# Kernel tuning notes

Measured on AMD Instinct MI355X. Metric: run time of the kernel, lower is better.

## Reference

```python
import jax, jax.numpy as jnp
import numpy as np

N = 10000
K1, K2 = 10, 25
DIM = 64
OUT = 128
NUM_GRAPHS = 64


def setup_inputs() -> dict:
    key = jax.random.key(0)
    ks = jax.random.split(key, 10)
    h0 = jax.random.normal(ks[0], (N, DIM), jnp.float32)
    h1 = jax.random.normal(ks[1], (N * K1, DIM), jnp.float32)
    h2 = jax.random.normal(ks[2], (N * K1 * K2, DIM), jnp.float32)
    # glorot-ish scaled weights
    w0 = jax.random.normal(ks[3], (2 * DIM, OUT), jnp.float32) * (2.0 / (2 * DIM + OUT)) ** 0.5
    b0 = jnp.zeros((OUT,), jnp.float32)
    w1 = jax.random.normal(ks[4], (2 * OUT, OUT), jnp.float32) * (2.0 / (3 * OUT)) ** 0.5
    b1 = jnp.zeros((OUT,), jnp.float32)
    wr1 = jax.random.normal(ks[5], (OUT, 35), jnp.float32) * (2.0 / (OUT + 35)) ** 0.5
    br1 = jnp.zeros((35,), jnp.float32)
    wr2 = jax.random.normal(ks[6], (35, 35), jnp.float32) * (2.0 / 70) ** 0.5
    br2 = jnp.zeros((35,), jnp.float32)
    wr3 = jax.random.normal(ks[7], (35, 1), jnp.float32) * (2.0 / 36) ** 0.5
    br3 = jnp.zeros((1,), jnp.float32)
    states_graph_ids = jnp.sort(jax.random.randint(ks[8], (N,), 0, NUM_GRAPHS, jnp.int32))
    return {
        "h0": h0, "h1": h1, "h2": h2,
        "w0": w0, "b0": b0, "w1": w1, "b1": b1,
        "wr1": wr1, "br1": br1, "wr2": wr2, "br2": br2, "wr3": wr3, "br3": br3,
        "states_graph_ids": states_graph_ids, "num_graphs": NUM_GRAPHS,
    }


def _aggr_mean(src, neigh, w, b):
    # GraphSAGE mean aggregator: concat(src, mean(neighbors)) @ w + b, relu
    n, d = src.shape
    k = neigh.shape[0] // n
    neigh_mean = neigh.reshape(n, k, d).mean(axis=1)  # (n, d)
    return jax.nn.relu(jnp.concatenate([src, neigh_mean], axis=1) @ w + b)


def reference(h0, h1, h2, w0, b0, w1, b1, wr1, br1, wr2, br2, wr3, br3,
              states_graph_ids, num_graphs):
    # round 0: shared aggregator across depths
    a01 = _aggr_mean(h0, h1, w0, b0)          # (N, OUT)
    a12 = _aggr_mean(h1, h2, w0, b0)          # (N*K1, OUT)
    # round 1
    out = _aggr_mean(a01, a12, w1, b1)        # (N, OUT)
    # segment_sum over sorted graph ids
    seg = jax.ops.segment_sum(out, states_graph_ids, num_segments=num_graphs,
                              indices_are_sorted=True)  # (G, OUT)
    # readout MLP (dropout inactive at inference)
    r = jax.nn.selu(seg @ wr1 + br1)
    r = jax.nn.selu(r @ wr2 + br2)
    r = r @ wr3 + br3                          # (G, 1)
    return r
```

## Files before the change

kernel.cpp:

```cpp
#include <hip/hip_runtime.h>
#include <hip/hip_bf16.h>
#include <math.h>

#define N_NODES 10000
#define K1 10
#define K2 25
#define DIM 64
#define OUT 128
#define NGRAPH 64

__global__ __launch_bounds__(256, 4) void kA(const float* __restrict__ h1,
                                             const float* __restrict__ h2,
                                             const float* __restrict__ w0,
                                             const float* __restrict__ b0,
                                             float* __restrict__ a12mean)
{
    __shared__ float  xbuf[K1][2 * DIM];
    __shared__ float4 red4[16][16];
    __shared__ float  pbuf[K1][OUT];

    const int t    = threadIdx.x;
    const int node = blockIdx.x;
    const int c    = t & 127;
    const int h    = t >> 7;

    float w0r[64];
#pragma unroll
    for (int k = 0; k < 64; ++k)
        w0r[k] = w0[(h * 64 + k) * OUT + c];
    const float b0r = b0[c];

    {
        const float* h1b = h1 + (size_t)node * (K1 * DIM);
        for (int idx = t; idx < K1 * DIM; idx += 256)
            xbuf[idx >> 6][idx & 63] = h1b[idx];
    }

    const int cc = t & 15;
    const int sl = t >> 4;
    const float4* h2b = (const float4*)h2 + (size_t)node * (K1 * K2 * DIM / 4);
    for (int j = 0; j < K1; ++j) {
        const float4* bj = h2b + j * (K2 * DIM / 4);
        float4 s = bj[sl * 16 + cc];
        if (sl < 9) {
            float4 s2 = bj[(sl + 16) * 16 + cc];
            s.x += s2.x; s.y += s2.y; s.z += s2.z; s.w += s2.w;
        }
        red4[sl][cc] = s;
        __syncthreads();
        if (t < 64) {
            const float* rf = (const float*)red4;
            float sum = 0.f;
#pragma unroll
            for (int ss = 0; ss < 16; ++ss) sum += rf[ss * 64 + t];
            xbuf[j][DIM + t] = sum * (1.0f / K2);
        }
        __syncthreads();
    }

    float myp[K1];
#pragma unroll
    for (int j = 0; j < K1; ++j) {
        const float4* xj = (const float4*)(&xbuf[j][h * DIM]);
        float p = 0.f;
#pragma unroll
        for (int k4 = 0; k4 < 16; ++k4) {
            float4 xv = xj[k4];
            p += xv.x * w0r[4 * k4 + 0];
            p += xv.y * w0r[4 * k4 + 1];
            p += xv.z * w0r[4 * k4 + 2];
            p += xv.w * w0r[4 * k4 + 3];
        }
        if (h == 1) pbuf[j][c] = p;
        else        myp[j]     = p;
    }
    __syncthreads();
    if (h == 0) {
        float acc = 0.f;
#pragma unroll
        for (int j = 0; j < K1; ++j) {
            float y = myp[j] + pbuf[j][c] + b0r;
            acc += (y > 0.f ? y : 0.f);
        }
        a12mean[(size_t)node * OUT + c] = acc * (1.0f / K1);
    }
}

__global__ __launch_bounds__(256, 2) void kB(const float* __restrict__ h0,
                                             const float* __restrict__ h1,
                                             const float* __restrict__ w0,
                                             const float* __restrict__ b0,
                                             const float* __restrict__ w1,
                                             const float* __restrict__ b1,
                                             const float* __restrict__ a12mean,
                                             const int*   __restrict__ gids,
                                             float* __restrict__ seg)
{
    __shared__ float x0[16][2 * DIM];
    __shared__ float x1[16][2 * OUT];
    __shared__ float pbuf[16][OUT];

    const int t  = threadIdx.x;
    const int n0 = blockIdx.x * 16;
    const int c  = t & 127;
    const int hh = t >> 7;

    float w0r[64];
#pragma unroll
    for (int k = 0; k < 64; ++k)
        w0r[k] = w0[(hh * 64 + k) * OUT + c];
    const float b0r = b0[c];

    for (int idx = t; idx < 16 * DIM; idx += 256)
        x0[idx >> 6][idx & 63] = h0[(size_t)n0 * DIM + idx];

    {
        const int col = t & 63, isub = t >> 6;
        for (int chunk = 0; chunk < 4; ++chunk) {
            const int il = chunk * 4 + isub;
            const float* b = h1 + (size_t)(n0 + il) * (K1 * DIM);
            float s = 0.f;
#pragma unroll
            for (int r = 0; r < K1; ++r) s += b[r * DIM + col];
            x0[il][DIM + col] = s * (1.0f / K1);
        }
    }

    for (int idx = t; idx < 16 * OUT; idx += 256)
        x1[idx >> 7][OUT + (idx & 127)] = a12mean[(size_t)n0 * OUT + idx];
    __syncthreads();

    float myp[16];
#pragma unroll
    for (int i = 0; i < 16; ++i) {
        const float4* xi = (const float4*)(&x0[i][hh * DIM]);
        float p = 0.f;
#pragma unroll
        for (int k4 = 0; k4 < 16; ++k4) {
            float4 xv = xi[k4];
            p += xv.x * w0r[4 * k4 + 0] + xv.y * w0r[4 * k4 + 1]
               + xv.z * w0r[4 * k4 + 2] + xv.w * w0r[4 * k4 + 3];
        }
        if (hh == 1) pbuf[i][c] = p; else myp[i] = p;
    }
    __syncthreads();
    if (hh == 0) {
#pragma unroll
        for (int i = 0; i < 16; ++i) {
            float y = myp[i] + pbuf[i][c] + b0r;
            x1[i][c] = (y > 0.f ? y : 0.f);
        }
    }

    float w1r[128];
#pragma unroll
    for (int k = 0; k < 128; ++k)
        w1r[k] = w1[(hh * 128 + k) * OUT + c];
    const float b1r = b1[c];
    __syncthreads();

#pragma unroll
    for (int i = 0; i < 16; ++i) {
        const float4* xi = (const float4*)(&x1[i][hh * OUT]);
        float p = 0.f;
#pragma unroll
        for (int k4 = 0; k4 < 32; ++k4) {
            float4 xv = xi[k4];
            p += xv.x * w1r[4 * k4 + 0] + xv.y * w1r[4 * k4 + 1]
               + xv.z * w1r[4 * k4 + 2] + xv.w * w1r[4 * k4 + 3];
        }
        if (hh == 1) pbuf[i][c] = p; else myp[i] = p;
    }
    __syncthreads();
    if (hh == 0) {
        int   runGid = gids[n0];
        float runSum = 0.f;
#pragma unroll
        for (int i = 0; i < 16; ++i) {
            float y = myp[i] + pbuf[i][c] + b1r;
            y = (y > 0.f ? y : 0.f);
            const int g = gids[n0 + i];
            if (g != runGid) {
                atomicAdd(&seg[runGid * OUT + c], runSum);
                runSum = 0.f; runGid = g;
            }
            runSum += y;
        }
        atomicAdd(&seg[runGid * OUT + c], runSum);
    }
}

__global__ void kC(const float* __restrict__ seg,
                   const float* __restrict__ wr1, const float* __restrict__ br1,
                   const float* __restrict__ wr2, const float* __restrict__ br2,
                   const float* __restrict__ wr3, const float* __restrict__ br3,
                   float* __restrict__ out)
{
    __shared__ float r1[35], r2[35];
    const int g = blockIdx.x, l = threadIdx.x;
    const float* s = seg + (size_t)g * OUT;
    const float SCALE = 1.0507009873554805f;
    const float ALPHA = 1.6732632423543772f;

    if (l < 35) {
        float d = br1[l];
        for (int k = 0; k < OUT; ++k) d += s[k] * wr1[k * 35 + l];
        r1[l] = d > 0.f ? SCALE * d : SCALE * ALPHA * (expf(d) - 1.f);
    }
    __syncthreads();
    if (l < 35) {
        float d = br2[l];
        for (int k = 0; k < 35; ++k) d += r1[k] * wr2[k * 35 + l];
        r2[l] = d > 0.f ? SCALE * d : SCALE * ALPHA * (expf(d) - 1.f);
    }
    __syncthreads();
    if (l == 0) {
        float d = br3[0];
        for (int k = 0; k < 35; ++k) d += r2[k] * wr3[k];
        out[g] = d;
    }
}

extern "C" void kernel_launch(void* const* d_in, const int* in_sizes, int n_in,
                              void* d_out, int out_size, void* d_ws, size_t ws_size,
                              hipStream_t stream)
{
    const float* h0  = (const float*)d_in[0];
    const float* h1  = (const float*)d_in[1];
    const float* h2  = (const float*)d_in[2];
    const float* w0  = (const float*)d_in[3];
    const float* b0  = (const float*)d_in[4];
    const float* w1  = (const float*)d_in[5];
    const float* b1  = (const float*)d_in[6];
    const float* wr1 = (const float*)d_in[7];
    const float* br1 = (const float*)d_in[8];
    const float* wr2 = (const float*)d_in[9];
    const float* br2 = (const float*)d_in[10];
    const float* wr3 = (const float*)d_in[11];
    const float* br3 = (const float*)d_in[12];
    const int*  gids = (const int*)d_in[13];

    float* a12mean = (float*)d_ws;
    float* seg     = a12mean + (size_t)N_NODES * OUT;
    float* out     = (float*)d_out;

    hipMemsetAsync(seg, 0, NGRAPH * OUT * sizeof(float), stream);
    kA<<<N_NODES, 256, 0, stream>>>(h1, h2, w0, b0, a12mean);
    kB<<<N_NODES / 16, 256, 0, stream>>>(h0, h1, w0, b0, w1, b1, a12mean, gids, seg);
    kC<<<NGRAPH, 64, 0, stream>>>(seg, wr1, br1, wr2, br2, wr3, br3, out);
}
```

Baseline: 925.9 us.

## Fuse both aggregation stages into one kernel with split-K register GEMV

```diff
diff --git a/kernel.cpp b/kernel.cpp
--- a/kernel.cpp
+++ b/kernel.cpp
@@ -1,5 +1,4 @@
 #include <hip/hip_runtime.h>
-#include <hip/hip_bf16.h>
 #include <math.h>
 
 #define N_NODES 10000
@@ -9,184 +8,157 @@
 #define OUT 128
 #define NGRAPH 64
 
-__global__ __launch_bounds__(256, 4) void kA(const float* __restrict__ h1,
-                                             const float* __restrict__ h2,
-                                             const float* __restrict__ w0,
-                                             const float* __restrict__ b0,
-                                             float* __restrict__ a12mean)
+#define NPB 2
+#define RPB (NPB * K1)
+#define XROWS (RPB + NPB)
+#define QP 36
+#define XPITCH (4 * QP)
+#define QP1 68
+#define X1PITCH (4 * QP1)
+
+__global__ __launch_bounds__(256, 4) void kFused(
+    const float* __restrict__ h0, const float* __restrict__ h1,
+    const float* __restrict__ h2, const float* __restrict__ w0,
+    const float* __restrict__ b0, const float* __restrict__ w1,
+    const float* __restrict__ b1, const int* __restrict__ gids,
+    float* __restrict__ seg)
 {
-    __shared__ float  xbuf[K1][2 * DIM];
-    __shared__ float4 red4[16][16];
-    __shared__ float  pbuf[K1][OUT];
-
-    const int t    = threadIdx.x;
-    const int node = blockIdx.x;
-    const int c    = t & 127;
-    const int h    = t >> 7;
-
-    float w0r[64];
-#pragma unroll
-    for (int k = 0; k < 64; ++k)
-        w0r[k] = w0[(h * 64 + k) * OUT + c];
-    const float b0r = b0[c];
-
-    {
-        const float* h1b = h1 + (size_t)node * (K1 * DIM);
-        for (int idx = t; idx < K1 * DIM; idx += 256)
-            xbuf[idx >> 6][idx & 63] = h1b[idx];
-    }
-
-    const int cc = t & 15;
-    const int sl = t >> 4;
-    const float4* h2b = (const float4*)h2 + (size_t)node * (K1 * K2 * DIM / 4);
-    for (int j = 0; j < K1; ++j) {
-        const float4* bj = h2b + j * (K2 * DIM / 4);
-        float4 s = bj[sl * 16 + cc];
-        if (sl < 9) {
-            float4 s2 = bj[(sl + 16) * 16 + cc];
-            s.x += s2.x; s.y += s2.y; s.z += s2.z; s.w += s2.w;
-        }
-        red4[sl][cc] = s;
-        __syncthreads();
-        if (t < 64) {
-            const float* rf = (const float*)red4;
-            float sum = 0.f;
-#pragma unroll
-            for (int ss = 0; ss < 16; ++ss) sum += rf[ss * 64 + t];
-            xbuf[j][DIM + t] = sum * (1.0f / K2);
-        }
-        __syncthreads();
-    }
-
-    float myp[K1];
-#pragma unroll
-    for (int j = 0; j < K1; ++j) {
-        const float4* xj = (const float4*)(&xbuf[j][h * DIM]);
-        float p = 0.f;
-#pragma unroll
-        for (int k4 = 0; k4 < 16; ++k4) {
-            float4 xv = xj[k4];
-            p += xv.x * w0r[4 * k4 + 0];
-            p += xv.y * w0r[4 * k4 + 1];
-            p += xv.z * w0r[4 * k4 + 2];
-            p += xv.w * w0r[4 * k4 + 3];
-        }
-        if (h == 1) pbuf[j][c] = p;
-        else        myp[j]     = p;
-    }
-    __syncthreads();
-    if (h == 0) {
-        float acc = 0.f;
-#pragma unroll
-        for (int j = 0; j < K1; ++j) {
-            float y = myp[j] + pbuf[j][c] + b0r;
-            acc += (y > 0.f ? y : 0.f);
-        }
-        a12mean[(size_t)node * OUT + c] = acc * (1.0f / K1);
-    }
-}
-
-__global__ __launch_bounds__(256, 2) void kB(const float* __restrict__ h0,
-                                             const float* __restrict__ h1,
-                                             const float* __restrict__ w0,
-                                             const float* __restrict__ b0,
-                                             const float* __restrict__ w1,
-                                             const float* __restrict__ b1,
-                                             const float* __restrict__ a12mean,
-                                             const int*   __restrict__ gids,
-                                             float* __restrict__ seg)
-{
-    __shared__ float x0[16][2 * DIM];
-    __shared__ float x1[16][2 * OUT];
-    __shared__ float pbuf[16][OUT];
+    __shared__ float xbuf[XROWS][XPITCH];
+    __shared__ float x1p[NPB][X1PITCH];
 
     const int t  = threadIdx.x;
-    const int n0 = blockIdx.x * 16;
-    const int c  = t & 127;
-    const int hh = t >> 7;
-
-    float w0r[64];
-#pragma unroll
-    for (int k = 0; k < 64; ++k)
-        w0r[k] = w0[(hh * 64 + k) * OUT + c];
-    const float b0r = b0[c];
-
-    for (int idx = t; idx < 16 * DIM; idx += 256)
-        x0[idx >> 6][idx & 63] = h0[(size_t)n0 * DIM + idx];
-
-    {
-        const int col = t & 63, isub = t >> 6;
-        for (int chunk = 0; chunk < 4; ++chunk) {
-            const int il = chunk * 4 + isub;
-            const float* b = h1 + (size_t)(n0 + il) * (K1 * DIM);
-            float s = 0.f;
-#pragma unroll
-            for (int r = 0; r < K1; ++r) s += b[r * DIM + col];
-            x0[il][DIM + col] = s * (1.0f / K1);
-        }
-    }
-
-    for (int idx = t; idx < 16 * OUT; idx += 256)
-        x1[idx >> 7][OUT + (idx & 127)] = a12mean[(size_t)n0 * OUT + idx];
-    __syncthreads();
-
-    float myp[16];
-#pragma unroll
-    for (int i = 0; i < 16; ++i) {
-        const float4* xi = (const float4*)(&x0[i][hh * DIM]);
-        float p = 0.f;
-#pragma unroll
-        for (int k4 = 0; k4 < 16; ++k4) {
-            float4 xv = xi[k4];
-            p += xv.x * w0r[4 * k4 + 0] + xv.y * w0r[4 * k4 + 1]
-               + xv.z * w0r[4 * k4 + 2] + xv.w * w0r[4 * k4 + 3];
-        }
-        if (hh == 1) pbuf[i][c] = p; else myp[i] = p;
-    }
-    __syncthreads();
-    if (hh == 0) {
-#pragma unroll
-        for (int i = 0; i < 16; ++i) {
-            float y = myp[i] + pbuf[i][c] + b0r;
-            x1[i][c] = (y > 0.f ? y : 0.f);
-        }
-    }
-
-    float w1r[128];
-#pragma unroll
-    for (int k = 0; k < 128; ++k)
-        w1r[k] = w1[(hh * 128 + k) * OUT + c];
-    const float b1r = b1[c];
-    __syncthreads();
-
-#pragma unroll
-    for (int i = 0; i < 16; ++i) {
-        const float4* xi = (const float4*)(&x1[i][hh * OUT]);
-        float p = 0.f;
-#pragma unroll
-        for (int k4 = 0; k4 < 32; ++k4) {
-            float4 xv = xi[k4];
-            p += xv.x * w1r[4 * k4 + 0] + xv.y * w1r[4 * k4 + 1]
-               + xv.z * w1r[4 * k4 + 2] + xv.w * w1r[4 * k4 + 3];
-        }
-        if (hh == 1) pbuf[i][c] = p; else myp[i] = p;
-    }
-    __syncthreads();
-    if (hh == 0) {
-        int   runGid = gids[n0];
-        float runSum = 0.f;
-#pragma unroll
-        for (int i = 0; i < 16; ++i) {
-            float y = myp[i] + pbuf[i][c] + b1r;
-            y = (y > 0.f ? y : 0.f);
-            const int g = gids[n0 + i];
-            if (g != runGid) {
-                atomicAdd(&seg[runGid * OUT + c], runSum);
-                runSum = 0.f; runGid = g;
+    const int w  = t >> 6;
+    const int l  = t & 63;
+    const int kq = l & 3;
+    const int cp = l >> 2;
+    const int c0 = w * 32 + cp * 2;
+    const int n0 = blockIdx.x * NPB;
+
+    float w0r0[32], w0r1[32];
+#pragma unroll
+    for (int kk = 0; kk < 32; ++kk) {
+        w0r0[kk] = w0[(kq * 32 + kk) * OUT + c0];
+        w0r1[kk] = w0[(kq * 32 + kk) * OUT + c0 + 1];
+    }
+    const float b00 = b0[c0], b01 = b0[c0 + 1];
+
+    if (t < NPB * DIM) {
+        const int i = t >> 6, cl = t & 63;
+        xbuf[RPB + i][(cl >> 5) * QP + (cl & 31)] = h0[(size_t)(n0 + i) * DIM + cl];
+    }
+
+#pragma unroll 1
+    for (int q = 0; q < 5; ++q) {
+        const int rloc = w + 4 * q;
+        const size_t rg = (size_t)n0 * K1 + rloc;
+        const float* hb = h2 + rg * (size_t)(K2 * DIM) + l;
+        float s = 0.f;
+#pragma unroll
+        for (int row = 0; row < K2; ++row)
+            s += __builtin_nontemporal_load(hb + row * DIM);
+        xbuf[rloc][(2 + (l >> 5)) * QP + (l & 31)] = s * (1.f / K2);
+        xbuf[rloc][(l >> 5) * QP + (l & 31)]       = h1[rg * DIM + l];
+    }
+    __syncthreads();
+
+    if (t < NPB * DIM) {
+        const int i = t >> 6, cl = t & 63;
+        float s = 0.f;
+#pragma unroll
+        for (int j = 0; j < K1; ++j)
+            s += xbuf[i * K1 + j][(cl >> 5) * QP + (cl & 31)];
+        xbuf[RPB + i][(2 + (cl >> 5)) * QP + (cl & 31)] = s * (1.f / K1);
+    }
+    __syncthreads();
+
+    float accA0 = 0.f, accA1 = 0.f, accB0 = 0.f, accB1 = 0.f;
+#pragma unroll 2
+    for (int j = 0; j < XROWS; ++j) {
+        const float4* xq = (const float4*)&xbuf[j][kq * QP];
+        float p0 = 0.f, p1 = 0.f;
+#pragma unroll
+        for (int m = 0; m < 8; ++m) {
+            const float4 x4 = xq[m];
+            p0 += x4.x * w0r0[4*m]   + x4.y * w0r0[4*m+1]
+                + x4.z * w0r0[4*m+2] + x4.w * w0r0[4*m+3];
+            p1 += x4.x * w0r1[4*m]   + x4.y * w0r1[4*m+1]
+                + x4.z * w0r1[4*m+2] + x4.w * w0r1[4*m+3];
+        }
+        p0 += __shfl_xor(p0, 1);  p0 += __shfl_xor(p0, 2);
+        p1 += __shfl_xor(p1, 1);  p1 += __shfl_xor(p1, 2);
+        const float y0 = fmaxf(p0 + b00, 0.f);
+        const float y1 = fmaxf(p1 + b01, 0.f);
+        if (j < K1)        { accA0 += y0; accA1 += y1; }
+        else if (j < RPB)  { accB0 += y0; accB1 += y1; }
+        else if (kq == 0) {
+            const int i = j - RPB;
+            float2* dst = (float2*)&x1p[i][(c0 >> 6) * QP1 + (c0 & 63)];
+            *dst = make_float2(y0, y1);
+        }
+    }
+    if (kq == 0) {
+        const int C = OUT + c0;
+        float2* d0 = (float2*)&x1p[0][(C >> 6) * QP1 + (C & 63)];
+        *d0 = make_float2(accA0 * (1.f / K1), accA1 * (1.f / K1));
+        float2* d1 = (float2*)&x1p[1][(C >> 6) * QP1 + (C & 63)];
+        *d1 = make_float2(accB0 * (1.f / K1), accB1 * (1.f / K1));
+    }
+    __syncthreads();
+
+    float pr00 = 0.f, pr01 = 0.f, pr10 = 0.f, pr11 = 0.f;
+#pragma unroll 1
+    for (int hh = 0; hh < 2; ++hh) {
+        float w1r0[32], w1r1[32];
+#pragma unroll
+        for (int kk = 0; kk < 32; ++kk) {
+            const int krow = kq * 64 + hh * 32 + kk;
+            w1r0[kk] = w1[krow * OUT + c0];
+            w1r1[kk] = w1[krow * OUT + c0 + 1];
+        }
+        {
+            const float4* xq = (const float4*)&x1p[0][kq * QP1 + hh * 32];
+            float p0 = 0.f, p1 = 0.f;
+#pragma unroll
+            for (int m = 0; m < 8; ++m) {
+                const float4 x4 = xq[m];
+                p0 += x4.x*w1r0[4*m] + x4.y*w1r0[4*m+1] + x4.z*w1r0[4*m+2] + x4.w*w1r0[4*m+3];
+                p1 += x4.x*w1r1[4*m] + x4.y*w1r1[4*m+1] + x4.z*w1r1[4*m+2] + x4.w*w1r1[4*m+3];
             }
-            runSum += y;
-        }
-        atomicAdd(&seg[runGid * OUT + c], runSum);
+            pr00 += p0; pr01 += p1;
+        }
+        {
+            const float4* xq = (const float4*)&x1p[1][kq * QP1 + hh * 32];
+            float p0 = 0.f, p1 = 0.f;
+#pragma unroll
+            for (int m = 0; m < 8; ++m) {
+                const float4 x4 = xq[m];
+                p0 += x4.x*w1r0[4*m] + x4.y*w1r0[4*m+1] + x4.z*w1r0[4*m+2] + x4.w*w1r0[4*m+3];
+                p1 += x4.x*w1r1[4*m] + x4.y*w1r1[4*m+1] + x4.z*w1r1[4*m+2] + x4.w*w1r1[4*m+3];
+            }
+            pr10 += p0; pr11 += p1;
+        }
+    }
+    const float b10 = b1[c0], b11 = b1[c0 + 1];
+    pr00 += __shfl_xor(pr00, 1); pr00 += __shfl_xor(pr00, 2);
+    pr01 += __shfl_xor(pr01, 1); pr01 += __shfl_xor(pr01, 2);
+    pr10 += __shfl_xor(pr10, 1); pr10 += __shfl_xor(pr10, 2);
+    pr11 += __shfl_xor(pr11, 1); pr11 += __shfl_xor(pr11, 2);
+    const float o00 = fmaxf(pr00 + b10, 0.f);
+    const float o01 = fmaxf(pr01 + b11, 0.f);
+    const float o10 = fmaxf(pr10 + b10, 0.f);
+    const float o11 = fmaxf(pr11 + b11, 0.f);
+
+    if (kq == 0) {
+        const int g0 = gids[n0], g1 = gids[n0 + 1];
+        if (g0 == g1) {
+            atomicAdd(&seg[g0 * OUT + c0],     o00 + o10);
+            atomicAdd(&seg[g0 * OUT + c0 + 1], o01 + o11);
+        } else {
+            atomicAdd(&seg[g0 * OUT + c0],     o00);
+            atomicAdd(&seg[g0 * OUT + c0 + 1], o01);
+            atomicAdd(&seg[g1 * OUT + c0],     o10);
+            atomicAdd(&seg[g1 * OUT + c0 + 1], o11);
+        }
     }
 }
 
@@ -240,12 +212,10 @@
     const float* br3 = (const float*)d_in[12];
     const int*  gids = (const int*)d_in[13];
 
-    float* a12mean = (float*)d_ws;
-    float* seg     = a12mean + (size_t)N_NODES * OUT;
-    float* out     = (float*)d_out;
+    float* seg = (float*)d_ws;
+    float* out = (float*)d_out;
 
     hipMemsetAsync(seg, 0, NGRAPH * OUT * sizeof(float), stream);
-    kA<<<N_NODES, 256, 0, stream>>>(h1, h2, w0, b0, a12mean);
-    kB<<<N_NODES / 16, 256, 0, stream>>>(h0, h1, w0, b0, w1, b1, a12mean, gids, seg);
+    kFused<<<N_NODES / NPB, 256, 0, stream>>>(h0, h1, h2, w0, b0, w1, b1, gids, seg);
     kC<<<NGRAPH, 64, 0, stream>>>(seg, wr1, br1, wr2, br2, wr3, br3, out);
 }
```

After: 1.005 ms. 8.6% more time.
